# Optimization experiments

Measured on AMD Instinct MI355X. Metric: run time of the kernel, lower is better.

## Reference

```python
import jax, jax.numpy as jnp
import numpy as np


def setup_inputs() -> dict:
    key = jax.random.key(0)
    ks = jax.random.split(key, 6)
    D, k, r = 4096, 16, 32  # embed_dim, low_rank_dimension, 2*low_rank_dimension
    B, S = 4, 4096
    return {
        "base": jax.random.normal(ks[0], (B, S, D), dtype=jnp.float32),
        "lora_A": jax.random.normal(ks[1], (k, D), dtype=jnp.float32),
        "lora_E": jax.random.normal(ks[2], (r, 1), dtype=jnp.float32),
        "lora_B": jax.random.normal(ks[3], (r, k), dtype=jnp.float32),
        "lora_aa": jax.random.normal(ks[4], (k, r), dtype=jnp.float32),
        "lora_bb": jax.random.normal(ks[5], (D, k), dtype=jnp.float32),
    }


def reference(base, lora_A, lora_E, lora_B, lora_aa, lora_bb):
    # Original math: base + base @ (A.T @ B.T @ diag(E) @ aa.T @ bb.T)
    #   result1 = A.T @ B.T  -> [D, r]
    #   result2 = aa.T @ bb.T -> [r, D]
    # Efficient equivalent: keep it low-rank; never build the [D, D] matrix
    # or the explicit diag. diag(E) @ result2 == E * result2 (row scaling).
    e = lora_E.reshape(-1)                              # [r]
    t = jnp.einsum('bsd,kd->bsk', base, lora_A)         # [B,S,k]  (base @ A.T)
    t = jnp.einsum('bsk,rk->bsr', t, lora_B)            # [B,S,r]  (.. @ B.T)
    t = t * e                                           # diag(E) scaling
    t = jnp.einsum('bsr,kr->bsk', t, lora_aa)           # [B,S,k]  (.. @ aa.T)
    delta = jnp.einsum('bsk,dk->bsd', t, lora_bb)       # [B,S,D]  (.. @ bb.T)
    return (base + delta).astype(base.dtype)
```

## Files before the change

kernel.cpp:

```cpp
#include <hip/hip_runtime.h>
#include <hip/hip_bf16.h>


#define D_DIM 4096
#define K_LR 16
#define R_LR 32
#define ROWS 64
#define DC 32
#define NSPLIT 4
#define DWIN 1024
#define WWIN 256
#define NCH (WWIN / DC)
#define NPART 16

typedef float f32x4 __attribute__((ext_vector_type(4)));

__global__ void __launch_bounds__(256) prep_kernel(const float* __restrict__ A,
                                                   const float* __restrict__ E,
                                                   const float* __restrict__ Bm,
                                                   const float* __restrict__ aa,
                                                   float* __restrict__ A2t) {
    __shared__ float Ms[K_LR][K_LR];
    const int t = threadIdx.x;
    {
        const int k = t >> 4, kp = t & 15;
        float s = 0.f;
        #pragma unroll
        for (int r = 0; r < R_LR; ++r)
            s += Bm[r * K_LR + k] * E[r] * aa[kp * R_LR + r];
        Ms[k][kp] = s;
    }
    __syncthreads();
    const int d = blockIdx.x * 256 + t;
    float acc[K_LR];
    #pragma unroll
    for (int kp = 0; kp < K_LR; ++kp) acc[kp] = 0.f;
    #pragma unroll
    for (int k = 0; k < K_LR; ++k) {
        const float a = A[k * D_DIM + d];
        #pragma unroll
        for (int kp = 0; kp < K_LR; ++kp) acc[kp] = fmaf(a, Ms[k][kp], acc[kp]);
    }
    #pragma unroll
    for (int kq = 0; kq < 4; ++kq) {
        f32x4 v = { acc[kq*4+0], acc[kq*4+1], acc[kq*4+2], acc[kq*4+3] };
        *(f32x4*)(A2t + (size_t)d * K_LR + kq * 4) = v;
    }
}

__global__ void __launch_bounds__(256) k1_kernel(const float* __restrict__ base,
                                                 const float* __restrict__ A2t,
                                                 float* __restrict__ Tp, int N) {
    __shared__ float stage[4][ROWS][DC];
    const int tid  = threadIdx.x;
    const int lane = tid & 63;
    const int wv   = __builtin_amdgcn_readfirstlane(tid >> 6);
    const int a    = lane >> 3;
    const int b    = lane & 7;
    const int rowtile = blockIdx.x / NSPLIT;
    const int split   = blockIdx.x % NSPLIT;
    const int r0 = rowtile * ROWS;
    const int d0 = split * DWIN + wv * WWIN;

    char* wbase = (char*)&stage[wv][0][0];
    const int swz_w = 16 * (b ^ a);
    const int swz_r = (lane & 7) << 4;

    float acc[K_LR];
    #pragma unroll
    for (int k = 0; k < K_LR; ++k) acc[k] = 0.f;

    f32x4 st[8];
    #pragma unroll
    for (int i = 0; i < 8; ++i)
        st[i] = *(const f32x4*)(base + (size_t)(r0 + i*8 + a) * D_DIM + d0 + 4*b);

    for (int c = 0; c < NCH; ++c) {
        #pragma unroll
        for (int i = 0; i < 8; ++i)
            *(f32x4*)(wbase + (i*8 + a) * 128 + swz_w) = st[i];
        if (c + 1 < NCH) {
            const int dcn = d0 + (c + 1) * DC;
            #pragma unroll
            for (int i = 0; i < 8; ++i)
                st[i] = *(const f32x4*)(base + (size_t)(r0 + i*8 + a) * D_DIM + dcn + 4*b);
        }
        const int dc = d0 + c * DC;
        #pragma unroll
        for (int j = 0; j < DC/4; ++j) {
            const f32x4 b4 = *(const f32x4*)(wbase + lane * 128 + ((16*j) ^ swz_r));
            const float* a2p = A2t + (size_t)(dc + 4*j) * K_LR;
            #pragma unroll
            for (int jj = 0; jj < 4; ++jj) {
                const float bv = b4[jj];
                #pragma unroll
                for (int k = 0; k < K_LR; ++k)
                    acc[k] = fmaf(bv, a2p[jj * K_LR + k], acc[k]);
            }
        }
    }
    const int ws = split * 4 + wv;
    float* tp = Tp + ((size_t)ws * N + r0 + lane) * K_LR;
    #pragma unroll
    for (int kq = 0; kq < 4; ++kq) {
        f32x4 v = { acc[kq*4+0], acc[kq*4+1], acc[kq*4+2], acc[kq*4+3] };
        *(f32x4*)(tp + kq * 4) = v;
    }
}

__global__ void __launch_bounds__(256) k1b_kernel(const float* __restrict__ Tp,
                                                  float* __restrict__ T, int N) {
    const int g = blockIdx.x * 256 + threadIdx.x;
    const size_t stride = (size_t)N * K_LR / 4;
    const f32x4* tp4 = (const f32x4*)Tp;
    f32x4 s = tp4[g];
    #pragma unroll
    for (int ws = 1; ws < NPART; ++ws)
        s += tp4[ws * stride + g];
    ((f32x4*)T)[g] = s;
}

__global__ void __launch_bounds__(256) k2_kernel(const float* __restrict__ base,
                                                 const float* __restrict__ bb,
                                                 const float* __restrict__ T,
                                                 float* __restrict__ out, int N) {
    const int tid  = threadIdx.x;
    const int lane = tid & 63;
    const int wv   = __builtin_amdgcn_readfirstlane(tid >> 6);
    const int rowtile = blockIdx.x >> 2;
    const int dwin    = blockIdx.x & 3;
    const int r0 = rowtile * ROWS;
    const int cbase = dwin * 1024 + wv * 256 + lane * 4;

    f32x4 bbr[4][4];
    #pragma unroll
    for (int q = 0; q < 4; ++q)
        #pragma unroll
        for (int kq = 0; kq < 4; ++kq)
            bbr[q][kq] = *(const f32x4*)(bb + (size_t)(cbase + q) * K_LR + kq * 4);

    #pragma unroll 2
    for (int r = 0; r < ROWS; ++r) {
        const size_t row = (size_t)(r0 + r);
        const float* tp = T + row * K_LR;
        float t16[K_LR];
        #pragma unroll
        for (int k = 0; k < K_LR; ++k) t16[k] = tp[k];

        const f32x4 bv = *(const f32x4*)(base + row * D_DIM + cbase);
        f32x4 ov;
        #pragma unroll
        for (int q = 0; q < 4; ++q) {
            float o = bv[q];
            #pragma unroll
            for (int k = 0; k < K_LR; ++k)
                o = fmaf(t16[k], bbr[q][k >> 2][k & 3], o);
            ov[q] = o;
        }
        __builtin_nontemporal_store(ov, (f32x4*)(out + row * D_DIM + cbase));
    }
}

extern "C" void kernel_launch(void* const* d_in, const int* in_sizes, int n_in,
                              void* d_out, int out_size, void* d_ws, size_t ws_size,
                              hipStream_t stream) {
    const float* base = (const float*)d_in[0];
    const float* A    = (const float*)d_in[1];
    const float* E    = (const float*)d_in[2];
    const float* Bm   = (const float*)d_in[3];
    const float* aa   = (const float*)d_in[4];
    const float* bb   = (const float*)d_in[5];
    float* out = (float*)d_out;
    const int N = in_sizes[0] / D_DIM;

    float* A2t = (float*)d_ws;
    float* Tp  = (float*)((char*)d_ws + (1u << 20));
    float* T   = (float*)((char*)d_ws + (32u << 20));

    prep_kernel<<<D_DIM / 256, 256, 0, stream>>>(A, E, Bm, aa, A2t);
    k1_kernel<<<(N / ROWS) * NSPLIT, 256, 0, stream>>>(base, A2t, Tp, N);
    k1b_kernel<<<(N * K_LR / 4) / 256, 256, 0, stream>>>(Tp, T, N);
    k2_kernel<<<(N / ROWS) * 4, 256, 0, stream>>>(base, bb, T, out, N);
}
```

Measured before the change: 164.6 us.

## Fuse reduction, partial-sum combine and output kernels into one row-tile kernel

Replaces the three-kernel pipeline (split-D partial reduction, partial-sum combine, output pass) with one kernel per 64-row tile of 512 threads. Eight waves each reduce a 512-wide slice of D, partials are summed in shared memory, and the block then writes the output for all of D in reverse order so recently loaded base data may still be cached. This removes the global partial-sum buffer traffic and two launches. In exchange the grid is far smaller, which cuts parallelism, and it relies on cache reuse of base.

```diff
diff --git a/kernel.cpp b/kernel.cpp
--- a/kernel.cpp
+++ b/kernel.cpp
@@ -6,12 +6,12 @@
 #define K_LR 16
 #define R_LR 32
 #define ROWS 64
+#define NW 8
+#define WWIN 512
 #define DC 32
-#define NSPLIT 4
-#define DWIN 1024
-#define WWIN 256
 #define NCH (WWIN / DC)
-#define NPART 16
+#define BWIN 2048
+#define NBW (D_DIM / BWIN)
 
 typedef float f32x4 __attribute__((ext_vector_type(4)));
 
@@ -48,116 +48,108 @@
     }
 }
 
-__global__ void __launch_bounds__(256) k1_kernel(const float* __restrict__ base,
-                                                 const float* __restrict__ A2t,
-                                                 float* __restrict__ Tp, int N) {
-    __shared__ float stage[4][ROWS][DC];
+__global__ void __launch_bounds__(512) fused_kernel(const float* __restrict__ base,
+                                                    const float* __restrict__ A2t,
+                                                    const float* __restrict__ bb,
+                                                    float* __restrict__ out, int N) {
+    __shared__ float stage[NW][ROWS][DC];
+    __shared__ float tred[ROWS][NW][K_LR];
+    __shared__ float tfin[ROWS][K_LR];
     const int tid  = threadIdx.x;
     const int lane = tid & 63;
     const int wv   = __builtin_amdgcn_readfirstlane(tid >> 6);
-    const int a    = lane >> 3;
-    const int b    = lane & 7;
-    const int rowtile = blockIdx.x / NSPLIT;
-    const int split   = blockIdx.x % NSPLIT;
-    const int r0 = rowtile * ROWS;
-    const int d0 = split * DWIN + wv * WWIN;
+    const int r0   = blockIdx.x * ROWS;
 
-    char* wbase = (char*)&stage[wv][0][0];
-    const int swz_w = 16 * (b ^ a);
-    const int swz_r = (lane & 7) << 4;
+    {
+        const int a = lane >> 3;
+        const int b = lane & 7;
+        const int d0 = wv * WWIN;
+        char* wbase = (char*)&stage[wv][0][0];
+        const int swz_w = 16 * (b ^ a);
+        const int swz_r = (lane & 7) << 4;
 
-    float acc[K_LR];
-    #pragma unroll
-    for (int k = 0; k < K_LR; ++k) acc[k] = 0.f;
+        float acc[K_LR];
+        #pragma unroll
+        for (int k = 0; k < K_LR; ++k) acc[k] = 0.f;
 
-    f32x4 st[8];
-    #pragma unroll
-    for (int i = 0; i < 8; ++i)
-        st[i] = *(const f32x4*)(base + (size_t)(r0 + i*8 + a) * D_DIM + d0 + 4*b);
-
-    for (int c = 0; c < NCH; ++c) {
+        f32x4 st[8];
         #pragma unroll
         for (int i = 0; i < 8; ++i)
-            *(f32x4*)(wbase + (i*8 + a) * 128 + swz_w) = st[i];
-        if (c + 1 < NCH) {
-            const int dcn = d0 + (c + 1) * DC;
+            st[i] = *(const f32x4*)(base + (size_t)(r0 + i*8 + a) * D_DIM + d0 + 4*b);
+
+        for (int c = 0; c < NCH; ++c) {
             #pragma unroll
             for (int i = 0; i < 8; ++i)
-                st[i] = *(const f32x4*)(base + (size_t)(r0 + i*8 + a) * D_DIM + dcn + 4*b);
+                *(f32x4*)(wbase + (i*8 + a) * 128 + swz_w) = st[i];
+            if (c + 1 < NCH) {
+                const int dcn = d0 + (c + 1) * DC;
+                #pragma unroll
+                for (int i = 0; i < 8; ++i)
+                    st[i] = *(const f32x4*)(base + (size_t)(r0 + i*8 + a) * D_DIM + dcn + 4*b);
+            }
+            const int dc = d0 + c * DC;
+            #pragma unroll
+            for (int j = 0; j < DC/4; ++j) {
+                const f32x4 b4 = *(const f32x4*)(wbase + lane * 128 + ((16*j) ^ swz_r));
+                const float* a2p = A2t + (size_t)(dc + 4*j) * K_LR;
+                #pragma unroll
+                for (int jj = 0; jj < 4; ++jj) {
+                    const float bv = b4[jj];
+                    #pragma unroll
+                    for (int k = 0; k < K_LR; ++k)
+                        acc[k] = fmaf(bv, a2p[jj * K_LR + k], acc[k]);
+                }
+            }
         }
-        const int dc = d0 + c * DC;
         #pragma unroll
-        for (int j = 0; j < DC/4; ++j) {
-            const f32x4 b4 = *(const f32x4*)(wbase + lane * 128 + ((16*j) ^ swz_r));
-            const float* a2p = A2t + (size_t)(dc + 4*j) * K_LR;
+        for (int kq = 0; kq < 4; ++kq) {
+            f32x4 v = { acc[kq*4+0], acc[kq*4+1], acc[kq*4+2], acc[kq*4+3] };
+            *(f32x4*)(&tred[lane][wv][kq * 4]) = v;
+        }
+    }
+    __syncthreads();
+    {
+        const int r = tid >> 3, kk = (tid & 7) * 2;
+        float s0 = 0.f, s1 = 0.f;
+        #pragma unroll
+        for (int w = 0; w < NW; ++w) {
+            s0 += tred[r][w][kk];
+            s1 += tred[r][w][kk + 1];
+        }
+        tfin[r][kk] = s0;
+        tfin[r][kk + 1] = s1;
+    }
+    __syncthreads();
+
+    for (int w = NBW - 1; w >= 0; --w) {
+        const int cbase = w * BWIN + tid * 4;
+        f32x4 bbr[4][4];
+        #pragma unroll
+        for (int q = 0; q < 4; ++q)
             #pragma unroll
-            for (int jj = 0; jj < 4; ++jj) {
-                const float bv = b4[jj];
+            for (int kq = 0; kq < 4; ++kq)
+                bbr[q][kq] = *(const f32x4*)(bb + (size_t)(cbase + q) * K_LR + kq * 4);
+
+        #pragma unroll 2
+        for (int r = 0; r < ROWS; ++r) {
+            f32x4 t16[4];
+            #pragma unroll
+            for (int kq = 0; kq < 4; ++kq)
+                t16[kq] = *(const f32x4*)(&tfin[r][kq * 4]);
+
+            const size_t row = (size_t)(r0 + r);
+            const f32x4 bv = *(const f32x4*)(base + row * D_DIM + cbase);
+            f32x4 ov;
+            #pragma unroll
+            for (int q = 0; q < 4; ++q) {
+                float o = bv[q];
                 #pragma unroll
                 for (int k = 0; k < K_LR; ++k)
-                    acc[k] = fmaf(bv, a2p[jj * K_LR + k], acc[k]);
+                    o = fmaf(t16[k >> 2][k & 3], bbr[q][k >> 2][k & 3], o);
+                ov[q] = o;
             }
+            __builtin_nontemporal_store(ov, (f32x4*)(out + row * D_DIM + cbase));
         }
-    }
-    const int ws = split * 4 + wv;
-    float* tp = Tp + ((size_t)ws * N + r0 + lane) * K_LR;
-    #pragma unroll
-    for (int kq = 0; kq < 4; ++kq) {
-        f32x4 v = { acc[kq*4+0], acc[kq*4+1], acc[kq*4+2], acc[kq*4+3] };
-        *(f32x4*)(tp + kq * 4) = v;
-    }
-}
-
-__global__ void __launch_bounds__(256) k1b_kernel(const float* __restrict__ Tp,
-                                                  float* __restrict__ T, int N) {
-    const int g = blockIdx.x * 256 + threadIdx.x;
-    const size_t stride = (size_t)N * K_LR / 4;
-    const f32x4* tp4 = (const f32x4*)Tp;
-    f32x4 s = tp4[g];
-    #pragma unroll
-    for (int ws = 1; ws < NPART; ++ws)
-        s += tp4[ws * stride + g];
-    ((f32x4*)T)[g] = s;
-}
-
-__global__ void __launch_bounds__(256) k2_kernel(const float* __restrict__ base,
-                                                 const float* __restrict__ bb,
-                                                 const float* __restrict__ T,
-                                                 float* __restrict__ out, int N) {
-    const int tid  = threadIdx.x;
-    const int lane = tid & 63;
-    const int wv   = __builtin_amdgcn_readfirstlane(tid >> 6);
-    const int rowtile = blockIdx.x >> 2;
-    const int dwin    = blockIdx.x & 3;
-    const int r0 = rowtile * ROWS;
-    const int cbase = dwin * 1024 + wv * 256 + lane * 4;
-
-    f32x4 bbr[4][4];
-    #pragma unroll
-    for (int q = 0; q < 4; ++q)
-        #pragma unroll
-        for (int kq = 0; kq < 4; ++kq)
-            bbr[q][kq] = *(const f32x4*)(bb + (size_t)(cbase + q) * K_LR + kq * 4);
-
-    #pragma unroll 2
-    for (int r = 0; r < ROWS; ++r) {
-        const size_t row = (size_t)(r0 + r);
-        const float* tp = T + row * K_LR;
-        float t16[K_LR];
-        #pragma unroll
-        for (int k = 0; k < K_LR; ++k) t16[k] = tp[k];
-
-        const f32x4 bv = *(const f32x4*)(base + row * D_DIM + cbase);
-        f32x4 ov;
-        #pragma unroll
-        for (int q = 0; q < 4; ++q) {
-            float o = bv[q];
-            #pragma unroll
-            for (int k = 0; k < K_LR; ++k)
-                o = fmaf(t16[k], bbr[q][k >> 2][k & 3], o);
-            ov[q] = o;
-        }
-        __builtin_nontemporal_store(ov, (f32x4*)(out + row * D_DIM + cbase));
     }
 }
 
@@ -174,11 +166,7 @@
     const int N = in_sizes[0] / D_DIM;
 
     float* A2t = (float*)d_ws;
-    float* Tp  = (float*)((char*)d_ws + (1u << 20));
-    float* T   = (float*)((char*)d_ws + (32u << 20));
 
     prep_kernel<<<D_DIM / 256, 256, 0, stream>>>(A, E, Bm, aa, A2t);
-    k1_kernel<<<(N / ROWS) * NSPLIT, 256, 0, stream>>>(base, A2t, Tp, N);
-    k1b_kernel<<<(N * K_LR / 4) / 256, 256, 0, stream>>>(Tp, T, N);
-    k2_kernel<<<(N / ROWS) * 4, 256, 0, stream>>>(base, bb, T, out, N);
+    fused_kernel<<<N / ROWS, 512, 0, stream>>>(base, A2t, bb, out, N);
 }
```

After: 174.7 us. 1.06x slower.
